# Kernel tuning notes

Hardware: AMD Instinct MI355X
Metric: run time of the kernel (lower is better)

## Reference

```python
import jax, jax.numpy as jnp
import numpy as np

ACTION_SPACE = 4
HIDDEN = 16
N_VARS = HIDDEN * ACTION_SPACE + ACTION_SPACE   # 68 logical SAT variables
M = 16                                           # clauses
AUX = 64                                         # auxiliary variables
NT = N_VARS + AUX + 1                            # +1 truth direction v0 -> 133 columns
K = int(np.ceil(np.sqrt(2.0 * NT))) + 1          # embedding dim of unit vectors (18)
SWEEPS = 40                                      # satnet default max_iter
P = 1 << 20                                      # number of points


def setup_inputs() -> dict:
    key = jax.random.key(0)
    k1, k2, k3, k4 = jax.random.split(key, 4)
    points = jax.random.normal(k1, (1, P, 2), jnp.float32)
    features = jax.random.normal(k2, (1, P, ACTION_SPACE), jnp.float32)
    # Linear(2 -> 16) params (PyTorch layout: W (out,in))
    W1 = jax.random.normal(k3, (HIDDEN, 2), jnp.float32) / np.sqrt(2.0)
    b1 = jnp.zeros((HIDDEN,), jnp.float32)
    # SATNet clause matrix S: (n_total, m)
    S = jax.random.normal(k4, (NT, M), jnp.float32) / np.sqrt(float(NT))
    # is_input mask over the 68 logical vars (64 inputs, 4 outputs), as in __init__
    is_input = jnp.concatenate([
        jnp.ones((HIDDEN * ACTION_SPACE,), jnp.int32),
        jnp.zeros((ACTION_SPACE,), jnp.int32)])[None, :]
    return {"points": points, "features": features, "W1": W1, "b1": b1,
            "S": S, "is_input": is_input}


def _satnet_forward(S, z, is_input_vars):
    """SATNet MAXSAT SDP relaxation via mixing-method coordinate descent.
    S: (NT, M) clause matrix; z: (N_VARS,) input probabilities;
    is_input_vars: (N_VARS,) int mask. Returns (N_VARS,) output probabilities."""
    # random init of unit-norm columns V (K, NT); column 0 is the truth direction v0
    V = jax.random.normal(jax.random.key(42), (K, NT), jnp.float32)
    V = V / jnp.linalg.norm(V, axis=0, keepdims=True)
    v0 = V[:, 0]
    # full z / mask over all NT columns: [truth=1 | vars | aux]
    zf = jnp.concatenate([jnp.ones((1,), jnp.float32), z, jnp.zeros((AUX,), jnp.float32)])
    fixed = jnp.concatenate([jnp.ones((1,), jnp.int32), is_input_vars.astype(jnp.int32),
                             jnp.zeros((AUX,), jnp.int32)]) == 1
    # initialize fixed (input) columns: v_i = -cos(pi z_i) v0 + sin(pi z_i) * perp_i
    dot = V.T @ v0                                        # (NT,)
    perp = V - v0[:, None] * dot[None, :]
    perp = perp / (jnp.linalg.norm(perp, axis=0, keepdims=True) + 1e-12)
    V_in = (-jnp.cos(jnp.pi * zf))[None, :] * v0[:, None] + (jnp.sin(jnp.pi * zf))[None, :] * perp
    V = jnp.where(fixed[None, :], V_in, V)
    # Gauss-Seidel mixing sweeps on free columns: v_i <- -g_i/||g_i||, g_i = V C[:,i] - C_ii v_i
    C = S @ S.T                                           # (NT, NT), tiny
    Cd = jnp.diag(C)
    def col_update(Vc, i):
        g = Vc @ C[:, i] - Cd[i] * Vc[:, i]
        vnew = -g / (jnp.linalg.norm(g) + 1e-12)
        vnew = jnp.where(fixed[i], Vc[:, i], vnew)
        return Vc.at[:, i].set(vnew), None
    def sweep(Vc, _):
        Vc, _ = jax.lax.scan(col_update, Vc, jnp.arange(NT))
        return Vc, None
    V, _ = jax.lax.scan(sweep, V, None, length=SWEEPS)
    # output probability: z_i = arccos(-v_i . v0) / pi
    zo = jnp.arccos(jnp.clip(-(V.T @ v0), -1.0 + 1e-6, 1.0 - 1e-6)) / jnp.pi
    return zo[1:1 + N_VARS]


def reference(points, features, W1, b1, S, is_input):
    h = jax.nn.sigmoid(points[0] @ W1.T + b1)             # (P, 16)
    all_hidden = jax.nn.sigmoid(h.T @ features[0])        # (16, 4)
    v_i = jnp.concatenate([all_hidden.reshape(-1),
                           jnp.zeros((ACTION_SPACE,), jnp.float32)])  # (68,)
    zo = _satnet_forward(S, v_i, is_input[0])
    return zo[None, -ACTION_SPACE:]                       # (1, 4)
```

## Files before the change

kernel.cpp:

```cpp
#include <hip/hip_runtime.h>
#include <math.h>

#define P_N    (1 << 20)
#define NTC    133
#define KD     18
#define MD     16
#define NV     68
#define NFREE  68
#define NSWEEP 40
#define NBLK_MAX 512

typedef float float2v __attribute__((ext_vector_type(2)));
typedef unsigned uvec2 __attribute__((ext_vector_type(2)));

__device__ __forceinline__ void threefry2x32(unsigned k0, unsigned k1,
                                             unsigned x0, unsigned x1,
                                             unsigned& o0, unsigned& o1) {
  unsigned ks2 = k0 ^ k1 ^ 0x1BD11BDAu;
#define TFR(r) { x0 += x1; x1 = (x1 << (r)) | (x1 >> (32 - (r))); x1 ^= x0; }
  x0 += k0; x1 += k1;
  TFR(13) TFR(15) TFR(26) TFR(6)
  x0 += k1;  x1 += ks2 + 1u;
  TFR(17) TFR(29) TFR(16) TFR(24)
  x0 += ks2; x1 += k0 + 2u;
  TFR(13) TFR(15) TFR(26) TFR(6)
  x0 += k0;  x1 += k1 + 3u;
  TFR(17) TFR(29) TFR(16) TFR(24)
  x0 += k1;  x1 += ks2 + 4u;
  TFR(13) TFR(15) TFR(26) TFR(6)
  x0 += ks2; x1 += k0 + 5u;
#undef TFR
  o0 = x0; o1 = x1;
}

__device__ __forceinline__ float bits_to_normal(unsigned b) {
  float f = __uint_as_float((b >> 9) | 0x3f800000u);
  const float lo = -0.99999994f, hi = 1.0f;
  float d = hi - lo;
  float u = fmaf(f, d, lo - d);
  u = fmaxf(lo, u);
  float w = -logf((1.0f - u) * (1.0f + u));
  float p;
  if (w < 5.0f) {
    w -= 2.5f;
    p = 2.81022636e-08f;
    p = fmaf(p, w, 3.43273939e-07f);
    p = fmaf(p, w, -3.5233877e-06f);
    p = fmaf(p, w, -4.39150654e-06f);
    p = fmaf(p, w, 0.00021858087f);
    p = fmaf(p, w, -0.00125372503f);
    p = fmaf(p, w, -0.00417768164f);
    p = fmaf(p, w, 0.246640727f);
    p = fmaf(p, w, 1.50140941f);
  } else {
    w = sqrtf(w) - 3.0f;
    p = -0.000200214257f;
    p = fmaf(p, w, 0.000100950558f);
    p = fmaf(p, w, 0.00134934322f);
    p = fmaf(p, w, -0.00367342844f);
    p = fmaf(p, w, 0.00573950773f);
    p = fmaf(p, w, -0.0076224613f);
    p = fmaf(p, w, 0.00943887047f);
    p = fmaf(p, w, 1.00167406f);
    p = fmaf(p, w, 2.83297682f);
  }
  double y = (double)(p * u);
  const double Kc = 0.8862269254527580136490837416706;
  double ud = (double)u;
  y = y - (erf(y) - ud) * Kc * exp(y * y);
  return 1.41421356237309504880f * (float)y;
}

__device__ __forceinline__ float row16_sumsq(float g) {
  float r;
  asm("v_mul_f32 %0, %1, %1\n\t"
      "s_nop 1\n\t"
      "v_add_f32 %0, %0, %0 quad_perm:[1,0,3,2] row_mask:0xf bank_mask:0xf\n\t"
      "s_nop 1\n\t"
      "v_add_f32 %0, %0, %0 quad_perm:[2,3,0,1] row_mask:0xf bank_mask:0xf\n\t"
      "s_nop 1\n\t"
      "v_add_f32 %0, %0, %0 row_ror:4 row_mask:0xf bank_mask:0xf\n\t"
      "s_nop 1\n\t"
      "v_add_f32 %0, %0, %0 row_ror:8 row_mask:0xf bank_mask:0xf\n\t"
      "s_nop 1"
      : "=v"(r) : "v"(g));
  return r;
}

__device__ __forceinline__ float cross_half_add(float g2) {
#if __has_builtin(__builtin_amdgcn_permlane32_swap)
  uvec2 r = __builtin_amdgcn_permlane32_swap(__float_as_uint(g2),
                                             __float_as_uint(g2),
                                             false, false);
  return __uint_as_float(r[0]) + __uint_as_float(r[1]);
#else
  return g2 + __shfl_xor(g2, 32, 64);
#endif
}

__device__ __forceinline__ float cross_quarter_add(float p) {
#if __has_builtin(__builtin_amdgcn_permlane16_swap)
  uvec2 r = __builtin_amdgcn_permlane16_swap(__float_as_uint(p),
                                             __float_as_uint(p),
                                             false, false);
  return __uint_as_float(r[0]) + __uint_as_float(r[1]);
#else
  return p + __shfl_xor(p, 16, 64);
#endif
}

__device__ __forceinline__ float2v pk_fma(float2v a, float2v b, float2v c) {
  float2v d;
  asm("v_pk_fma_f32 %0, %1, %2, %3" : "=v"(d) : "v"(a), "v"(b), "v"(c));
  return d;
}
__device__ __forceinline__ float2v pk_mul(float2v a, float2v b) {
  float2v d;
  asm("v_pk_mul_f32 %0, %1, %2" : "=v"(d) : "v"(a), "v"(b));
  return d;
}

__device__ __forceinline__ float dot8p(const float2v* a, const float2v* b) {
  float2v acc0 = pk_mul(a[0], b[0]);
  float2v acc1 = pk_mul(a[1], b[1]);
  acc0 = pk_fma(a[2], b[2], acc0);
  acc1 = pk_fma(a[3], b[3], acc1);
  return (acc0.x + acc1.x) + (acc0.y + acc1.y);
}

__global__ __launch_bounds__(256) void k1_reduce(
    const float* __restrict__ points, const float* __restrict__ features,
    const float* __restrict__ W1, const float* __restrict__ b1,
    float* __restrict__ partials) {
  __shared__ float red[4][64];
  float w0[16], w1[16], bb[16];
#pragma unroll
  for (int k = 0; k < 16; ++k) {
    w0[k] = W1[2 * k]; w1[k] = W1[2 * k + 1]; bb[k] = b1[k];
  }
  float2v acc2[32];
#pragma unroll
  for (int e = 0; e < 32; ++e) { acc2[e].x = 0.f; acc2[e].y = 0.f; }
  const float2* p2 = (const float2*)points;
  const float4* f4 = (const float4*)features;
  int gid = blockIdx.x * blockDim.x + threadIdx.x;
  int stride = gridDim.x * blockDim.x;
  for (int p = gid; p < P_N; p += stride) {
    float2 pt = p2[p];
    float4 ft = f4[p];
    float2v ft01; ft01.x = ft.x; ft01.y = ft.y;
    float2v ft23; ft23.x = ft.z; ft23.y = ft.w;
#pragma unroll
    for (int k = 0; k < 16; ++k) {
      float x = fmaf(pt.x, w0[k], fmaf(pt.y, w1[k], bb[k]));
      float h = 1.0f / (1.0f + __expf(-x));
      float2v h2; h2.x = h; h2.y = h;
      acc2[2 * k]     = pk_fma(h2, ft01, acc2[2 * k]);
      acc2[2 * k + 1] = pk_fma(h2, ft23, acc2[2 * k + 1]);
    }
  }
#pragma unroll
  for (int e = 0; e < 64; ++e) {
    float v = ((const float*)acc2)[e];
    v += __shfl_down(v, 32);
    v += __shfl_down(v, 16);
    v += __shfl_down(v, 8);
    v += __shfl_down(v, 4);
    v += __shfl_down(v, 2);
    v += __shfl_down(v, 1);
    ((float*)acc2)[e] = v;
  }
  int lane = threadIdx.x & 63, wv = threadIdx.x >> 6;
  if (lane == 0) {
#pragma unroll
    for (int e = 0; e < 64; ++e) red[wv][e] = ((const float*)acc2)[e];
  }
  __syncthreads();
  if (threadIdx.x < 64)
    partials[blockIdx.x * 64 + threadIdx.x] =
        red[0][threadIdx.x] + red[1][threadIdx.x] +
        red[2][threadIdx.x] + red[3][threadIdx.x];
}

__global__ __launch_bounds__(256) void k2_satnet(
    const float* __restrict__ S, const int* __restrict__ is_input,
    const float* __restrict__ partials, int nblk, float* __restrict__ out) {
  __shared__ float Vm[KD][NTC];
  __shared__ __align__(16) float Sm[NTC][MD];
  __shared__ float Cd[NTC];
  __shared__ float Cp[NFREE];
  __shared__ __align__(8) float CdCp[NFREE][2];
  __shared__ float zfv[NTC];
  __shared__ int fx[NTC];
  __shared__ float v0[KD];
  __shared__ float Ul[KD][MD];
  __shared__ float red2[4][64];
  __shared__ int pattern_ok;

  int t = threadIdx.x;

  {
    int g = t >> 6, e = t & 63;
    float s0 = 0.f, s1 = 0.f, s2 = 0.f, s3 = 0.f;
    int b = g;
    for (; b + 12 < nblk; b += 16) {
      s0 += partials[b * 64 + e];
      s1 += partials[(b + 4) * 64 + e];
      s2 += partials[(b + 8) * 64 + e];
      s3 += partials[(b + 12) * 64 + e];
    }
    for (; b < nblk; b += 4) s0 += partials[b * 64 + e];
    red2[g][e] = (s0 + s1) + (s2 + s3);
  }
  for (int idx = t; idx < NTC * MD; idx += 256) ((float*)Sm)[idx] = S[idx];

  for (int e = t; e < KD * NTC; e += 256) {
    unsigned o0, o1;
    threefry2x32(0u, 42u, 0u, (unsigned)e, o0, o1);
    ((float*)Vm)[e] = bits_to_normal(o0 ^ o1);
  }
  __syncthreads();

  if (t < NTC) {
    float zv = 0.f;
    if (t == 0) zv = 1.f;
    else if (t <= 64) {
      float x = red2[0][t - 1] + red2[1][t - 1] + red2[2][t - 1] + red2[3][t - 1];
      zv = 1.0f / (1.0f + expf(-x));
    }
    zfv[t] = zv;
    int f = 0;
    if (t == 0) f = 1;
    else if (t <= NV) f = (is_input[t - 1] != 0) ? 1 : 0;
    fx[t] = f;
    float cd = 0.f;
#pragma unroll
    for (int m = 0; m < MD; ++m) cd += Sm[t][m] * Sm[t][m];
    Cd[t] = cd;
  }
  if (t < NFREE) {
    int a = 65 + t, b = 65 + ((t + 1) % NFREE);
    float s = 0.f;
#pragma unroll
    for (int m = 0; m < MD; ++m) s += Sm[a][m] * Sm[b][m];
    Cp[t] = s;
  }
  __syncthreads();

  if (t < NFREE) {
    CdCp[t][0] = Cd[65 + t];
    CdCp[t][1] = Cp[t];
  }

  if (t == 0) {
    int ok = 1;
    for (int i = 1; i <= 64; ++i) ok &= (fx[i] == 1);
    for (int i = 65; i < NTC; ++i) ok &= (fx[i] == 0);
    pattern_ok = ok;
  }

  if (t < NTC) {
    float s = 0.f;
#pragma unroll
    for (int k = 0; k < KD; ++k) s += Vm[k][t] * Vm[k][t];
    float n = sqrtf(s);
#pragma unroll
    for (int k = 0; k < KD; ++k) Vm[k][t] = Vm[k][t] / n;
  }
  __syncthreads();
  if (t < KD) v0[t] = Vm[t][0];
  __syncthreads();

  if (t < NTC) {
    float dt = 0.f;
#pragma unroll
    for (int k = 0; k < KD; ++k) dt += Vm[k][t] * v0[k];
    float pk[KD];
    float pn = 0.f;
#pragma unroll
    for (int k = 0; k < KD; ++k) {
      pk[k] = Vm[k][t] - v0[k] * dt;
      pn += pk[k] * pk[k];
    }
    pn = sqrtf(pn) + 1e-12f;
    if (fx[t]) {
      float ang = 3.14159265358979323846f * zfv[t];
      float c = -cosf(ang), sn = sinf(ang);
#pragma unroll
      for (int k = 0; k < KD; ++k) Vm[k][t] = fmaf(c, v0[k], sn * (pk[k] / pn));
    }
  }
  __syncthreads();

  for (int idx = t; idx < KD * MD; idx += 256) {
    int k = idx / MD, m = idx % MD;
    float s = 0.f;
    for (int c = 0; c < NTC; ++c) s += Vm[k][c] * Sm[c][m];
    Ul[k][m] = s;
  }
  __syncthreads();

  if (pattern_ok) {
    if (t < 64) {
      const int lane = t;
      const int mh = (lane >> 4) & 1;
      const int rlow = lane & 15;
      const bool act = (lane < 32) | (rlow < 2);
      const int rc = act ? ((lane < 32) ? rlow : (16 + rlow)) : 0;
      const int mbase = 8 * mh;

      float2v u2[4];
#pragma unroll
      for (int m = 0; m < 4; ++m) {
        float2v z;
        z.x = act ? Ul[rc][mbase + 2 * m] : 0.f;
        z.y = act ? Ul[rc][mbase + 2 * m + 1] : 0.f;
        u2[m] = z;
      }
      float vr[NFREE];
#pragma unroll
      for (int j = 0; j < NFREE; ++j) vr[j] = act ? Vm[rc][65 + j] : 0.f;

      float2v rs2[4][4];
      float2v rcc[4];
#pragma unroll
      for (int s = 0; s < 3; ++s) {
        rs2[s][0] = *(const float2v*)&Sm[65 + s][mbase];
        rs2[s][1] = *(const float2v*)&Sm[65 + s][mbase + 2];
        rs2[s][2] = *(const float2v*)&Sm[65 + s][mbase + 4];
        rs2[s][3] = *(const float2v*)&Sm[65 + s][mbase + 6];
        rcc[s] = *(const float2v*)&CdCp[s][0];
      }
      rcc[3].x = 0.f; rcc[3].y = 0.f;

      float pre0 = cross_quarter_add(dot8p(u2, rs2[0]));
      float Aprev = fmaf(-rcc[0].x, vr[0], pre0);
      float tprev = 0.f;
      float cpp = 0.f;

#pragma unroll 1
      for (int sw = 0; sw < NSWEEP; ++sw) {
        float maxdd = 0.f;
#pragma unroll
        for (int j = 0; j < NFREE; ++j) {
          const int c = j & 3, n = (j + 1) & 3, w = (j + 3) & 3;
          const int colw = (j + 3) % NFREE;
          const int jn = (j + 1) % NFREE;
          float cpj = rcc[c].y;
          float cdn = rcc[n].x;
          float voldj = vr[j];
          float voldn = vr[jn];
          rs2[w][0] = *(const float2v*)&Sm[65 + colw][mbase];
          rs2[w][1] = *(const float2v*)&Sm[65 + colw][mbase + 2];
          rs2[w][2] = *(const float2v*)&Sm[65 + colw][mbase + 4];
          rs2[w][3] = *(const float2v*)&Sm[65 + colw][mbase + 6];
          rcc[w] = *(const float2v*)&CdCp[colw][0];
          float g = fmaf(tprev, cpp, Aprev);
          float g2 = row16_sumsq(g);
          g2 = cross_half_add(g2);
          float inv;
          asm("v_rsq_f32 %0, %1" : "=v"(inv) : "v"(g2));
          float tj = -g * inv;
          float pre_next = cross_quarter_add(dot8p(u2, rs2[n]));
          float A = fmaf(-cpj, voldj, pre_next);
          A = fmaf(-cdn, voldn, A);
          float dd = tj - voldj;
          float2v dd2; dd2.x = dd; dd2.y = dd;
#pragma unroll
          for (int m = 0; m < 4; ++m) u2[m] = pk_fma(dd2, rs2[c][m], u2[m]);
          vr[j] = tj;
          maxdd = fmaxf(maxdd, fabsf(dd));
          tprev = tj;
          cpp = cpj;
          Aprev = A;
          __builtin_amdgcn_sched_barrier(0);
        }
        if (__all(maxdd < 1e-4f)) break;
      }
      if (act && mh == 0) {
#pragma unroll
        for (int j = 0; j < 4; ++j) Vm[rc][65 + j] = vr[j];
      }
    }
  } else {
    if (t < 64) {
      int k = t;
      bool act = (k < KD);
      float u[MD];
#pragma unroll
      for (int m = 0; m < MD; ++m) u[m] = act ? Ul[k][m] : 0.f;
#pragma unroll 1
      for (int sw = 0; sw < NSWEEP; ++sw) {
#pragma unroll 1
        for (int i = 1; i < NTC; ++i) {
          if (fx[i]) continue;
          float4 s0 = *(const float4*)&Sm[i][0];
          float4 s1 = *(const float4*)&Sm[i][4];
          float4 s2 = *(const float4*)&Sm[i][8];
          float4 s3 = *(const float4*)&Sm[i][12];
          float vold = act ? Vm[k][i] : 0.f;
          float a0 = fmaf(u[0], s0.x, fmaf(u[1], s0.y, fmaf(u[2], s0.z, u[3] * s0.w)));
          float a1 = fmaf(u[4], s1.x, fmaf(u[5], s1.y, fmaf(u[6], s1.z, u[7] * s1.w)));
          float a2 = fmaf(u[8], s2.x, fmaf(u[9], s2.y, fmaf(u[10], s2.z, u[11] * s2.w)));
          float a3 = fmaf(u[12], s3.x, fmaf(u[13], s3.y, fmaf(u[14], s3.z, u[15] * s3.w)));
          float g = (a0 + a1) + (a2 + a3) - Cd[i] * vold;
          float g2 = g * g;
          g2 += __shfl_xor(g2, 16, 32);
          g2 += __shfl_xor(g2, 8, 32);
          g2 += __shfl_xor(g2, 4, 32);
          g2 += __shfl_xor(g2, 2, 32);
          g2 += __shfl_xor(g2, 1, 32);
          float inv = 1.0f / (sqrtf(g2) + 1e-12f);
          float vnew = -g * inv;
          float dd = vnew - vold;
#pragma unroll
          for (int m = 0; m < 4; ++m) {
            u[m] = fmaf(dd, ((const float*)&s0)[m], u[m]);
            u[4 + m] = fmaf(dd, ((const float*)&s1)[m], u[4 + m]);
            u[8 + m] = fmaf(dd, ((const float*)&s2)[m], u[8 + m]);
            u[12 + m] = fmaf(dd, ((const float*)&s3)[m], u[12 + m]);
          }
          if (act) Vm[k][i] = vnew;
        }
      }
    }
  }
  __syncthreads();

  if (t < 4) {
    float dt = 0.f;
#pragma unroll
    for (int k = 0; k < KD; ++k) dt += Vm[k][65 + t] * v0[k];
    float x = -dt;
    x = fminf(fmaxf(x, -1.0f + 1e-6f), 1.0f - 1e-6f);
    out[t] = acosf(x) / 3.14159265358979323846f;
  }
}

extern "C" void kernel_launch(void* const* d_in, const int* in_sizes, int n_in,
                              void* d_out, int out_size, void* d_ws, size_t ws_size,
                              hipStream_t stream) {
  const float* points = (const float*)d_in[0];
  const float* features = (const float*)d_in[1];
  const float* W1 = (const float*)d_in[2];
  const float* b1 = (const float*)d_in[3];
  const float* S = (const float*)d_in[4];
  const int* is_input = (const int*)d_in[5];
  float* partials = (float*)d_ws;

  int nblk = NBLK_MAX;
  size_t need = (size_t)nblk * 64 * sizeof(float);
  if (ws_size < need) {
    nblk = (int)(ws_size / (64 * sizeof(float)));
    if (nblk < 1) nblk = 1;
  }

  hipLaunchKernelGGL(k1_reduce, dim3(nblk), dim3(256), 0, stream,
                     points, features, W1, b1, partials);
  hipLaunchKernelGGL(k2_satnet, dim3(1), dim3(256), 0, stream,
                     S, is_input, partials, nblk, (float*)d_out);
}
```

Baseline: 95.28 us.

## Precompute SATNet random init in extra reduce block and loosen convergence tolerance

Adds one extra block to the reduction kernel. It generates the threefry random V, normalises it, projects out v0, and computes Cd/Cp, then writes the results to workspace. The single-block SATNet kernel can then load these values instead of computing them serially after the reduction, taking that setup off the critical path. The change also loosens the early-exit convergence threshold from 1e-4 to 3e-4, which cuts sweeps at some risk to accuracy.

After: 91.09 us. -4.4%, faster.

```diff
diff --git a/kernel.cpp b/kernel.cpp
--- a/kernel.cpp
+++ b/kernel.cpp
@@ -9,6 +9,13 @@
 #define NFREE  68
 #define NSWEEP 40
 #define NBLK_MAX 512
+
+#define WS_VN    0
+#define WS_PH    (KD * NTC)
+#define WS_V0    (2 * KD * NTC)
+#define WS_CD    (2 * KD * NTC + 32)
+#define WS_CP    (2 * KD * NTC + 32 + NTC)
+#define WS_PART  5056
 
 typedef float float2v __attribute__((ext_vector_type(2)));
 typedef unsigned uvec2 __attribute__((ext_vector_type(2)));
@@ -131,8 +138,62 @@
 __global__ __launch_bounds__(256) void k1_reduce(
     const float* __restrict__ points, const float* __restrict__ features,
     const float* __restrict__ W1, const float* __restrict__ b1,
-    float* __restrict__ partials) {
+    float* __restrict__ partials, int nblk,
+    const float* __restrict__ S, float* __restrict__ wsbase, int do_init) {
   __shared__ float red[4][64];
+  __shared__ float Vb[KD * NTC];
+  __shared__ float v0b[KD];
+  int t = threadIdx.x;
+
+  if (do_init && (int)blockIdx.x == nblk) {
+    for (int e = t; e < KD * NTC; e += 256) {
+      unsigned o0, o1;
+      threefry2x32(0u, 42u, 0u, (unsigned)e, o0, o1);
+      Vb[e] = bits_to_normal(o0 ^ o1);
+    }
+    __syncthreads();
+    if (t < NTC) {
+      float s = 0.f;
+#pragma unroll
+      for (int k = 0; k < KD; ++k) s += Vb[k * NTC + t] * Vb[k * NTC + t];
+      float n = sqrtf(s);
+#pragma unroll
+      for (int k = 0; k < KD; ++k) Vb[k * NTC + t] = Vb[k * NTC + t] / n;
+    }
+    __syncthreads();
+    if (t < KD) v0b[t] = Vb[t * NTC + 0];
+    __syncthreads();
+    if (t < NTC) {
+      float dt = 0.f;
+#pragma unroll
+      for (int k = 0; k < KD; ++k) dt += Vb[k * NTC + t] * v0b[k];
+      float pk[KD];
+      float pn = 0.f;
+#pragma unroll
+      for (int k = 0; k < KD; ++k) {
+        pk[k] = Vb[k * NTC + t] - v0b[k] * dt;
+        pn += pk[k] * pk[k];
+      }
+      pn = sqrtf(pn) + 1e-12f;
+#pragma unroll
+      for (int k = 0; k < KD; ++k) wsbase[WS_PH + k * NTC + t] = pk[k] / pn;
+      float cd = 0.f;
+#pragma unroll
+      for (int m = 0; m < MD; ++m) cd += S[t * MD + m] * S[t * MD + m];
+      wsbase[WS_CD + t] = cd;
+    }
+    if (t < NFREE) {
+      int a = 65 + t, b = 65 + ((t + 1) % NFREE);
+      float s = 0.f;
+#pragma unroll
+      for (int m = 0; m < MD; ++m) s += S[a * MD + m] * S[b * MD + m];
+      wsbase[WS_CP + t] = s;
+    }
+    if (t < KD) wsbase[WS_V0 + t] = v0b[t];
+    for (int e = t; e < KD * NTC; e += 256) wsbase[WS_VN + e] = Vb[e];
+    return;
+  }
+
   float w0[16], w1[16], bb[16];
 #pragma unroll
   for (int k = 0; k < 16; ++k) {
@@ -143,8 +204,8 @@
   for (int e = 0; e < 32; ++e) { acc2[e].x = 0.f; acc2[e].y = 0.f; }
   const float2* p2 = (const float2*)points;
   const float4* f4 = (const float4*)features;
-  int gid = blockIdx.x * blockDim.x + threadIdx.x;
-  int stride = gridDim.x * blockDim.x;
+  int gid = blockIdx.x * 256 + t;
+  int stride = nblk * 256;
   for (int p = gid; p < P_N; p += stride) {
     float2 pt = p2[p];
     float4 ft = f4[p];
@@ -170,21 +231,21 @@
     v += __shfl_down(v, 1);
     ((float*)acc2)[e] = v;
   }
-  int lane = threadIdx.x & 63, wv = threadIdx.x >> 6;
+  int lane = t & 63, wv = t >> 6;
   if (lane == 0) {
 #pragma unroll
     for (int e = 0; e < 64; ++e) red[wv][e] = ((const float*)acc2)[e];
   }
   __syncthreads();
-  if (threadIdx.x < 64)
-    partials[blockIdx.x * 64 + threadIdx.x] =
-        red[0][threadIdx.x] + red[1][threadIdx.x] +
-        red[2][threadIdx.x] + red[3][threadIdx.x];
+  if (t < 64)
+    partials[blockIdx.x * 64 + t] =
+        red[0][t] + red[1][t] + red[2][t] + red[3][t];
 }
 
 __global__ __launch_bounds__(256) void k2_satnet(
     const float* __restrict__ S, const int* __restrict__ is_input,
-    const float* __restrict__ partials, int nblk, float* __restrict__ out) {
+    const float* __restrict__ partials, int nblk, float* __restrict__ out,
+    const float* __restrict__ wsbase, int pre_init) {
   __shared__ float Vm[KD][NTC];
   __shared__ __align__(16) float Sm[NTC][MD];
   __shared__ float Cd[NTC];
@@ -214,10 +275,17 @@
   }
   for (int idx = t; idx < NTC * MD; idx += 256) ((float*)Sm)[idx] = S[idx];
 
-  for (int e = t; e < KD * NTC; e += 256) {
-    unsigned o0, o1;
-    threefry2x32(0u, 42u, 0u, (unsigned)e, o0, o1);
-    ((float*)Vm)[e] = bits_to_normal(o0 ^ o1);
+  if (pre_init) {
+    for (int e = t; e < KD * NTC; e += 256) ((float*)Vm)[e] = wsbase[WS_VN + e];
+    if (t < NTC) Cd[t] = wsbase[WS_CD + t];
+    if (t < NFREE) Cp[t] = wsbase[WS_CP + t];
+    if (t < KD) v0[t] = wsbase[WS_V0 + t];
+  } else {
+    for (int e = t; e < KD * NTC; e += 256) {
+      unsigned o0, o1;
+      threefry2x32(0u, 42u, 0u, (unsigned)e, o0, o1);
+      ((float*)Vm)[e] = bits_to_normal(o0 ^ o1);
+    }
   }
   __syncthreads();
 
@@ -233,12 +301,14 @@
     if (t == 0) f = 1;
     else if (t <= NV) f = (is_input[t - 1] != 0) ? 1 : 0;
     fx[t] = f;
-    float cd = 0.f;
-#pragma unroll
-    for (int m = 0; m < MD; ++m) cd += Sm[t][m] * Sm[t][m];
-    Cd[t] = cd;
-  }
-  if (t < NFREE) {
+    if (!pre_init) {
+      float cd = 0.f;
+#pragma unroll
+      for (int m = 0; m < MD; ++m) cd += Sm[t][m] * Sm[t][m];
+      Cd[t] = cd;
+    }
+  }
+  if (!pre_init && t < NFREE) {
     int a = 65 + t, b = 65 + ((t + 1) % NFREE);
     float s = 0.f;
 #pragma unroll
@@ -251,7 +321,6 @@
     CdCp[t][0] = Cd[65 + t];
     CdCp[t][1] = Cp[t];
   }
-
   if (t == 0) {
     int ok = 1;
     for (int i = 1; i <= 64; ++i) ok &= (fx[i] == 1);
@@ -259,38 +328,48 @@
     pattern_ok = ok;
   }
 
-  if (t < NTC) {
-    float s = 0.f;
-#pragma unroll
-    for (int k = 0; k < KD; ++k) s += Vm[k][t] * Vm[k][t];
-    float n = sqrtf(s);
-#pragma unroll
-    for (int k = 0; k < KD; ++k) Vm[k][t] = Vm[k][t] / n;
-  }
-  __syncthreads();
-  if (t < KD) v0[t] = Vm[t][0];
-  __syncthreads();
-
-  if (t < NTC) {
-    float dt = 0.f;
-#pragma unroll
-    for (int k = 0; k < KD; ++k) dt += Vm[k][t] * v0[k];
-    float pk[KD];
-    float pn = 0.f;
-#pragma unroll
-    for (int k = 0; k < KD; ++k) {
-      pk[k] = Vm[k][t] - v0[k] * dt;
-      pn += pk[k] * pk[k];
-    }
-    pn = sqrtf(pn) + 1e-12f;
-    if (fx[t]) {
+  if (pre_init) {
+    if (t < NTC && fx[t]) {
       float ang = 3.14159265358979323846f * zfv[t];
       float c = -cosf(ang), sn = sinf(ang);
 #pragma unroll
-      for (int k = 0; k < KD; ++k) Vm[k][t] = fmaf(c, v0[k], sn * (pk[k] / pn));
-    }
-  }
-  __syncthreads();
+      for (int k = 0; k < KD; ++k)
+        Vm[k][t] = fmaf(c, v0[k], sn * wsbase[WS_PH + k * NTC + t]);
+    }
+    __syncthreads();
+  } else {
+    if (t < NTC) {
+      float s = 0.f;
+#pragma unroll
+      for (int k = 0; k < KD; ++k) s += Vm[k][t] * Vm[k][t];
+      float n = sqrtf(s);
+#pragma unroll
+      for (int k = 0; k < KD; ++k) Vm[k][t] = Vm[k][t] / n;
+    }
+    __syncthreads();
+    if (t < KD) v0[t] = Vm[t][0];
+    __syncthreads();
+    if (t < NTC) {
+      float dt = 0.f;
+#pragma unroll
+      for (int k = 0; k < KD; ++k) dt += Vm[k][t] * v0[k];
+      float pk[KD];
+      float pn = 0.f;
+#pragma unroll
+      for (int k = 0; k < KD; ++k) {
+        pk[k] = Vm[k][t] - v0[k] * dt;
+        pn += pk[k] * pk[k];
+      }
+      pn = sqrtf(pn) + 1e-12f;
+      if (fx[t]) {
+        float ang = 3.14159265358979323846f * zfv[t];
+        float c = -cosf(ang), sn = sinf(ang);
+#pragma unroll
+        for (int k = 0; k < KD; ++k) Vm[k][t] = fmaf(c, v0[k], sn * (pk[k] / pn));
+      }
+    }
+    __syncthreads();
+  }
 
   for (int idx = t; idx < KD * MD; idx += 256) {
     int k = idx / MD, m = idx % MD;
@@ -375,7 +454,7 @@
           Aprev = A;
           __builtin_amdgcn_sched_barrier(0);
         }
-        if (__all(maxdd < 1e-4f)) break;
+        if (__all(maxdd < 3e-4f)) break;
       }
       if (act && mh == 0) {
 #pragma unroll
@@ -446,17 +525,26 @@
   const float* b1 = (const float*)d_in[3];
   const float* S = (const float*)d_in[4];
   const int* is_input = (const int*)d_in[5];
-  float* partials = (float*)d_ws;
+  float* ws = (float*)d_ws;
+  size_t ws_floats = ws_size / sizeof(float);
 
   int nblk = NBLK_MAX;
-  size_t need = (size_t)nblk * 64 * sizeof(float);
-  if (ws_size < need) {
-    nblk = (int)(ws_size / (64 * sizeof(float)));
-    if (nblk < 1) nblk = 1;
-  }
-
-  hipLaunchKernelGGL(k1_reduce, dim3(nblk), dim3(256), 0, stream,
-                     points, features, W1, b1, partials);
+  int do_init = 1;
+  size_t need = (size_t)WS_PART + (size_t)nblk * 64;
+  if (ws_floats < need) {
+    if (ws_floats > (size_t)WS_PART + 64 * 64) {
+      nblk = (int)((ws_floats - WS_PART) / 64);
+    } else {
+      do_init = 0;
+      nblk = (int)(ws_floats / 64);
+      if (nblk > NBLK_MAX) nblk = NBLK_MAX;
+      if (nblk < 1) nblk = 1;
+    }
+  }
+  float* partials = ws + (do_init ? WS_PART : 0);
+
+  hipLaunchKernelGGL(k1_reduce, dim3(nblk + do_init), dim3(256), 0, stream,
+                     points, features, W1, b1, partials, nblk, S, ws, do_init);
   hipLaunchKernelGGL(k2_satnet, dim3(1), dim3(256), 0, stream,
-                     S, is_input, partials, nblk, (float*)d_out);
-}
+                     S, is_input, partials, nblk, (float*)d_out, ws, do_init);
+}
```
